# Kernel tuning notes

Hardware: AMD Instinct MI355X
Metric: run time of the kernel (lower is better)

The kernel has to match this reference:

```python
import jax, jax.numpy as jnp
import numpy as np

SAMPLE_RATE = 32000.0
NUM_APPLICATIONS = 3


def _eq_biquad(x, freq, gain, q, sr):
    """torchaudio.functional.equalizer_biquad: peaking EQ biquad + lfilter.
    x: [B, T] float; freq/gain/q: scalars.
    """
    w0 = 2.0 * jnp.pi * freq / sr
    A = jnp.exp(gain / 40.0 * jnp.log(10.0))  # 10 ** (gain / 40)
    alpha = jnp.sin(w0) / (2.0 * q)
    b0 = 1.0 + alpha * A
    b1 = -2.0 * jnp.cos(w0)
    b2 = 1.0 - alpha * A
    a0 = 1.0 + alpha / A
    a1 = -2.0 * jnp.cos(w0)
    a2 = 1.0 - alpha / A
    # normalize by a0 (as torchaudio biquad -> lfilter does)
    b0, b1, b2 = b0 / a0, b1 / a0, b2 / a0
    a1, a2 = a1 / a0, a2 / a0

    B = x.shape[0]
    z = jnp.zeros((B,), x.dtype)

    def step(carry, xn):
        x1, x2, y1, y2 = carry
        yn = b0 * xn + b1 * x1 + b2 * x2 - a1 * y1 - a2 * y2
        return (xn, x1, yn, y1), yn

    # scan over time axis; carry is per-batch state vectors
    _, y = jax.lax.scan(step, (z, z, z, z), x.T)  # y: [T, B]
    return y.T


def setup_inputs() -> dict:
    key = jax.random.key(0)
    k1, k2, k3, k4 = jax.random.split(key, 4)
    clip = jax.random.normal(k1, (128, 160000), dtype=jnp.float32)
    # draws within the module's f/g/q ranges
    freqs = jax.random.uniform(k2, (NUM_APPLICATIONS,), jnp.float32, 100.0, 6000.0)
    gains = jax.random.uniform(k3, (NUM_APPLICATIONS,), jnp.float32, -8.0, 8.0)
    qs = jax.random.uniform(k4, (NUM_APPLICATIONS,), jnp.float32, 1.0, 9.0)
    return {"clip": clip, "freqs": freqs, "gains": gains, "qs": qs}


def reference(clip, freqs, gains, qs):
    x = clip
    for i in range(NUM_APPLICATIONS):
        x = _eq_biquad(x, freqs[i], gains[i], qs[i], SAMPLE_RATE)
    return x
```

## Files before the change

### kernel.cpp

```cpp
#include <hip/hip_runtime.h>
#include <math.h>

#define SRATE 32000.f
#define NB 128
#define NT 160000
#define CL 50
#define CPB 128
#define NCROW 3200
#define NTILE 3200
#define TPR 25
#define SEG 50
#define LROW 52
#define RECROW (NCROW*8)

#ifndef M_PI
#define M_PI 3.14159265358979323846
#endif

__device__ __forceinline__ void coeffs_f32(
    const float* fr, const float* gn, const float* qs, float* c)
{
  #pragma unroll
  for (int f = 0; f < 3; ++f) {
    float w0 = 2.f * (float)M_PI * fr[f] / SRATE;
    float A  = expf(gn[f] * (2.302585093f / 40.f));
    float al = sinf(w0) / (2.f * qs[f]);
    float cw = cosf(w0);
    float a0 = 1.f + al / A;
    c[f*5+0] = (1.f + al*A) / a0;
    c[f*5+1] = -2.f * cw / a0;
    c[f*5+2] = (1.f - al*A) / a0;
    c[f*5+3] = -2.f * cw / a0;
    c[f*5+4] = (1.f - al/A) / a0;
  }
}


__global__ __launch_bounds__(128) void eq_a(
    const float* __restrict__ x, const float* __restrict__ fr,
    const float* __restrict__ gn, const float* __restrict__ qs,
    float* __restrict__ eoT)
{
  __shared__ float lds[CPB * LROW];
  const int tid = threadIdx.x;
  const int t = blockIdx.x;
  float c[15];
  coeffs_f32(fr, gn, qs, c);
  const float* xg = x + (size_t)t * (CPB * CL);
  #pragma unroll
  for (int it = 0; it < 25; ++it) {
    int f = it * 128 + tid;
    int seg = f / 25, off = f % 25;
    float2 v = *(const float2*)(xg + seg*CL + off*2);
    int pos = off + seg; pos -= (pos >= 25) ? 25 : 0; pos -= (pos >= 25) ? 25 : 0;
    pos = (off + seg) % 25;
    *(float2*)(&lds[seg*LROW + pos*2]) = v;
  }
  __syncthreads();
  const int gci = t * CPB + tid;
  const int ci  = gci % NCROW;
  float x1, x2;
  if (tid == 0) {
    if (ci == 0) { x1 = 0.f; x2 = 0.f; }
    else { x1 = xg[-1]; x2 = xg[-2]; }
  } else {
    const int ps = tid - 1;
    const int pp = (ps + 24) % 25;
    x1 = lds[ps*LROW + pp*2 + 1];
    x2 = lds[ps*LROW + pp*2 + 0];
  }
  float y1p=0,y1pp=0,y2p=0,y2pp=0,y3p=0,y3pp=0;
  int rr = tid % 25;
  #pragma unroll
  for (int jj = 0; jj < 25; ++jj) {
    float2 xv = *(const float2*)(&lds[tid*LROW + rr*2]);
    rr = (rr == 24) ? 0 : rr + 1;
    #pragma unroll
    for (int q = 0; q < 2; ++q) {
      const float xn = q ? xv.y : xv.x;
      float y1 = c[0]*xn + c[1]*x1  + c[2]*x2   - c[3]*y1p  - c[4]*y1pp;
      float y2 = c[5]*y1 + c[6]*y1p + c[7]*y1pp - c[8]*y2p  - c[9]*y2pp;
      float y3 = c[10]*y2 + c[11]*y2p + c[12]*y2pp - c[13]*y3p - c[14]*y3pp;
      x2=x1; x1=xn;
      y1pp=y1p; y1p=y1; y2pp=y2p; y2p=y2; y3pp=y3p; y3p=y3;
    }
  }
  const int row = gci / NCROW;
  const int plane = ci % SEG, slot = ci / SEG;
  float* ep = eoT + (size_t)row * RECROW + ((size_t)plane*64 + slot)*8;
  float4 r0; r0.x=y1p; r0.y=y1pp; r0.z=y2p; r0.w=y2pp;
  float4 r1; r1.x=y3p; r1.y=y3pp; r1.z=0.f; r1.w=0.f;
  *(float4*)ep = r0; *(float4*)(ep+4) = r1;
}

__global__ __launch_bounds__(64) void eq_b(
    const float* __restrict__ fr, const float* __restrict__ gn,
    const float* __restrict__ qs, const float* __restrict__ eoT,
    float* __restrict__ sgD)
{
  __shared__ double Mb[36], Rb[36], Tb[36];
  __shared__ float Hs[36], Gs[6*36];
  const int l = threadIdx.x, row = blockIdx.x;
  float c[15];
  coeffs_f32(fr, gn, qs, c);
  if (l < 6) {
    double s0=0,s1=0,s2=0,s3=0,s4=0,s5=0;
    if (l==0) s0=1; else if (l==1) s1=1; else if (l==2) s2=1;
    else if (l==3) s3=1; else if (l==4) s4=1; else s5=1;
    double y1 = -(double)c[3]*s0 - (double)c[4]*s1;
    double y2 = (double)c[5]*y1 + (double)c[6]*s0 + (double)c[7]*s1
              - (double)c[8]*s2 - (double)c[9]*s3;
    double y3 = (double)c[10]*y2 + (double)c[11]*s2 + (double)c[12]*s3
              - (double)c[13]*s4 - (double)c[14]*s5;
    Mb[0*6+l]=y1; Mb[1*6+l]=s0; Mb[2*6+l]=y2; Mb[3*6+l]=s2; Mb[4*6+l]=y3; Mb[5*6+l]=s4;
  }
  if (l < 36) Rb[l] = ((l % 7) == 0) ? 1.0 : 0.0;
  __syncthreads();
  const int i = l / 6, j = l % 6;
  int e = CL;
  while (e) {
    if (e & 1) {
      double acc = 0.0;
      if (l < 36) { for (int k = 0; k < 6; ++k) acc += Rb[i*6+k]*Mb[k*6+j]; Tb[l]=acc; }
      __syncthreads();
      if (l < 36) Rb[l] = Tb[l];
      __syncthreads();
    }
    e >>= 1;
    if (e) {
      double acc = 0.0;
      if (l < 36) { for (int k = 0; k < 6; ++k) acc += Mb[i*6+k]*Mb[k*6+j]; Tb[l]=acc; }
      __syncthreads();
      if (l < 36) Mb[l] = Tb[l];
      __syncthreads();
    }
  }
  if (l < 36) { Hs[l] = (float)Rb[l]; Mb[l] = Rb[l]; }
  __syncthreads();
  if (l < 36) Rb[l] = ((l % 7) == 0) ? 1.0 : 0.0;
  __syncthreads();
  e = SEG;
  while (e) {
    if (e & 1) {
      double acc = 0.0;
      if (l < 36) { for (int k = 0; k < 6; ++k) acc += Rb[i*6+k]*Mb[k*6+j]; Tb[l]=acc; }
      __syncthreads();
      if (l < 36) Rb[l] = Tb[l];
      __syncthreads();
    }
    e >>= 1;
    if (e) {
      double acc = 0.0;
      if (l < 36) { for (int k = 0; k < 6; ++k) acc += Mb[i*6+k]*Mb[k*6+j]; Tb[l]=acc; }
      __syncthreads();
      if (l < 36) Mb[l] = Tb[l];
      __syncthreads();
    }
  }
  if (l < 36) Gs[l] = (float)Rb[l];
  __syncthreads();
  for (int k = 1; k < 6; ++k) {
    double acc = 0.0;
    if (l < 36) { for (int m = 0; m < 6; ++m) acc += Rb[i*6+m]*Rb[m*6+j]; Tb[l]=acc; }
    __syncthreads();
    if (l < 36) Rb[l] = Tb[l];
    __syncthreads();
    if (l < 36) Gs[k*36+l] = (float)Rb[l];
    __syncthreads();
  }

  float H[36];
  #pragma unroll
  for (int q = 0; q < 36; ++q) H[q] = Hs[q];
  const float* rbase = eoT + (size_t)row * RECROW;
  float u[6] = {0,0,0,0,0,0};
  for (int jj = 0; jj < SEG; ++jj) {
    const float* ep = rbase + ((size_t)jj*64 + l)*8;
    float4 r0 = *(const float4*)ep, r1 = *(const float4*)(ep+4);
    float ev[6] = {r0.x,r0.y,r0.z,r0.w,r1.x,r1.y};
    float nu[6];
    #pragma unroll
    for (int q = 0; q < 6; ++q) {
      float a = ev[q];
      #pragma unroll
      for (int m = 0; m < 6; ++m) a += H[q*6+m]*u[m];
      nu[q] = a;
    }
    #pragma unroll
    for (int q = 0; q < 6; ++q) u[q] = nu[q];
  }
  float v6[6];
  #pragma unroll
  for (int q = 0; q < 6; ++q) v6[q] = u[q];
  #pragma unroll
  for (int k = 0; k < 6; ++k) {
    const float* G = Gs + k*36;
    float o[6];
    #pragma unroll
    for (int q = 0; q < 6; ++q) o[q] = __shfl_up(v6[q], 1u << k, 64);
    if (l >= (1 << k)) {
      float nv[6];
      #pragma unroll
      for (int q = 0; q < 6; ++q) {
        float a = v6[q];
        #pragma unroll
        for (int m = 0; m < 6; ++m) a += G[q*6+m]*o[m];
        nv[q] = a;
      }
      #pragma unroll
      for (int q = 0; q < 6; ++q) v6[q] = nv[q];
    }
  }
  float s[6];
  #pragma unroll
  for (int q = 0; q < 6; ++q) s[q] = __shfl_up(v6[q], 1, 64);
  if (l == 0) {
    #pragma unroll
    for (int q = 0; q < 6; ++q) s[q] = 0.f;
  }
  float* wbase = sgD + (size_t)row * RECROW;
  for (int jj = 0; jj < SEG; ++jj) {
    const float* ep = rbase + ((size_t)jj*64 + l)*8;
    float4 r0 = *(const float4*)ep, r1 = *(const float4*)(ep+4);
    float ev[6] = {r0.x,r0.y,r0.z,r0.w,r1.x,r1.y};
    float* wp = wbase + ((size_t)l*SEG + jj)*8;
    float4 w0; w0.x=s[0]; w0.y=s[1]; w0.z=s[2]; w0.w=s[3];
    float4 w1; w1.x=s[4]; w1.y=s[5]; w1.z=0.f; w1.w=0.f;
    *(float4*)wp = w0; *(float4*)(wp+4) = w1;
    float ns[6];
    #pragma unroll
    for (int q = 0; q < 6; ++q) {
      float a = ev[q];
      #pragma unroll
      for (int m = 0; m < 6; ++m) a += H[q*6+m]*s[m];
      ns[q] = a;
    }
    #pragma unroll
    for (int q = 0; q < 6; ++q) s[q] = ns[q];
  }
}

__global__ __launch_bounds__(128) void eq_c(
    const float* __restrict__ x, const float* __restrict__ fr,
    const float* __restrict__ gn, const float* __restrict__ qs,
    const float* __restrict__ sgD, float* __restrict__ y)
{
  __shared__ float lds[CPB * LROW];
  const int tid = threadIdx.x;
  const int t = blockIdx.x;
  float c[15];
  coeffs_f32(fr, gn, qs, c);
  const float* xg = x + (size_t)t * (CPB * CL);
  float* yg = y + (size_t)t * (CPB * CL);
  #pragma unroll
  for (int it = 0; it < 25; ++it) {
    int f = it * 128 + tid;
    int seg = f / 25, off = f % 25;
    float2 v = *(const float2*)(xg + seg*CL + off*2);
    int pos = (off + seg) % 25;
    *(float2*)(&lds[seg*LROW + pos*2]) = v;
  }
  __syncthreads();
  const int gci = t * CPB + tid;
  const int ci  = gci % NCROW;
  float x1, x2;
  if (tid == 0) {
    if (ci == 0) { x1 = 0.f; x2 = 0.f; }
    else { x1 = xg[-1]; x2 = xg[-2]; }
  } else {
    const int ps = tid - 1;
    const int pp = (ps + 24) % 25;
    x1 = lds[ps*LROW + pp*2 + 1];
    x2 = lds[ps*LROW + pp*2 + 0];
  }
  __syncthreads();
  const int row = gci / NCROW;
  const float* sp = sgD + (size_t)row * RECROW + (size_t)ci * 8;
  float4 s0 = *(const float4*)sp, s1 = *(const float4*)(sp+4);
  float y1p=s0.x, y1pp=s0.y, y2p=s0.z, y2pp=s0.w, y3p=s1.x, y3pp=s1.y;
  int rr = tid % 25;
  #pragma unroll
  for (int jj = 0; jj < 25; ++jj) {
    float2 xv = *(const float2*)(&lds[tid*LROW + rr*2]);
    float2 yv;
    #pragma unroll
    for (int q = 0; q < 2; ++q) {
      const float xn = q ? xv.y : xv.x;
      float y1 = c[0]*xn + c[1]*x1  + c[2]*x2   - c[3]*y1p  - c[4]*y1pp;
      float y2 = c[5]*y1 + c[6]*y1p + c[7]*y1pp - c[8]*y2p  - c[9]*y2pp;
      float y3 = c[10]*y2 + c[11]*y2p + c[12]*y2pp - c[13]*y3p - c[14]*y3pp;
      x2=x1; x1=xn;
      y1pp=y1p; y1p=y1; y2pp=y2p; y2p=y2; y3pp=y3p; y3p=y3;
      if (q) yv.y = y3; else yv.x = y3;
    }
    *(float2*)(&lds[tid*LROW + rr*2]) = yv;
    rr = (rr == 24) ? 0 : rr + 1;
  }
  __syncthreads();
  #pragma unroll
  for (int it = 0; it < 25; ++it) {
    int f = it * 128 + tid;
    int seg = f / 25, off = f % 25;
    int pos = (off + seg) % 25;
    float2 v = *(const float2*)(&lds[seg*LROW + pos*2]);
    *(float2*)(yg + seg*CL + off*2) = v;
  }
}

extern "C" void kernel_launch(void* const* d_in, const int* in_sizes, int n_in,
                              void* d_out, int out_size, void* d_ws, size_t ws_size,
                              hipStream_t stream) {
  const float* clip = (const float*)d_in[0];
  const float* fr   = (const float*)d_in[1];
  const float* gn   = (const float*)d_in[2];
  const float* qs   = (const float*)d_in[3];
  float* out = (float*)d_out;
  float* eoT = (float*)d_ws;
  float* sgD = eoT + (size_t)NB * RECROW;

  eq_a<<<NTILE, 128, 0, stream>>>(clip, fr, gn, qs, eoT);
  eq_b<<<NB, 64, 0, stream>>>(fr, gn, qs, eoT, sgD);
  eq_c<<<NTILE, 128, 0, stream>>>(clip, fr, gn, qs, sgD, out);
}
```

Measured before the change: 90.61 us.

## Persistent grid with double-buffered async global-to-LDS staging in scan kernels

Converts the two per-chunk IIR kernels into persistent kernels over a fixed grid that loop over tiles. Each next tile is prefetched into a second LDS buffer with direct global-to-LDS loads while the current tile is filtered. The swizzled padded LDS layout is replaced by a plain contiguous layout, and neighbour history is obtained with a wavefront shuffle instead of LDS reads. This aims to hide global load latency and cut staging instruction overhead, at the cost of possible LDS bank conflicts and reliance on correct async-load synchronization.

```diff
diff --git a/kernel.cpp b/kernel.cpp
--- a/kernel.cpp
+++ b/kernel.cpp
@@ -10,7 +10,8 @@
 #define NTILE 3200
 #define TPR 25
 #define SEG 50
-#define LROW 52
+#define TILEF 6400
+#define GRID 768
 #define RECROW (NCROW*8)
 
 #ifndef M_PI
@@ -35,62 +36,74 @@
   }
 }
 
+__device__ __forceinline__ void stage_half(
+    const float* __restrict__ src0, float* dst0, int lane)
+{
+  const float* src = src0 + lane * 4;
+  #pragma unroll
+  for (int cc = 0; cc < 12; ++cc) {
+    __builtin_amdgcn_global_load_lds(
+        (const __attribute__((address_space(1))) void*)(src + cc*256),
+        (__attribute__((address_space(3))) void*)(dst0 + cc*256), 16, 0, 0);
+  }
+  if (lane < 32) {
+    __builtin_amdgcn_global_load_lds(
+        (const __attribute__((address_space(1))) void*)(src + 12*256),
+        (__attribute__((address_space(3))) void*)(dst0 + 12*256), 16, 0, 0);
+  }
+}
 
 __global__ __launch_bounds__(128) void eq_a(
     const float* __restrict__ x, const float* __restrict__ fr,
     const float* __restrict__ gn, const float* __restrict__ qs,
     float* __restrict__ eoT)
 {
-  __shared__ float lds[CPB * LROW];
-  const int tid = threadIdx.x;
-  const int t = blockIdx.x;
+  __shared__ float lds[2][TILEF];
+  const int tid = threadIdx.x, lane = tid & 63, wave = tid >> 6;
   float c[15];
   coeffs_f32(fr, gn, qs, c);
-  const float* xg = x + (size_t)t * (CPB * CL);
-  #pragma unroll
-  for (int it = 0; it < 25; ++it) {
-    int f = it * 128 + tid;
-    int seg = f / 25, off = f % 25;
-    float2 v = *(const float2*)(xg + seg*CL + off*2);
-    int pos = off + seg; pos -= (pos >= 25) ? 25 : 0; pos -= (pos >= 25) ? 25 : 0;
-    pos = (off + seg) % 25;
-    *(float2*)(&lds[seg*LROW + pos*2]) = v;
-  }
-  __syncthreads();
-  const int gci = t * CPB + tid;
-  const int ci  = gci % NCROW;
-  float x1, x2;
-  if (tid == 0) {
-    if (ci == 0) { x1 = 0.f; x2 = 0.f; }
-    else { x1 = xg[-1]; x2 = xg[-2]; }
-  } else {
-    const int ps = tid - 1;
-    const int pp = (ps + 24) % 25;
-    x1 = lds[ps*LROW + pp*2 + 1];
-    x2 = lds[ps*LROW + pp*2 + 0];
-  }
-  float y1p=0,y1pp=0,y2p=0,y2pp=0,y3p=0,y3pp=0;
-  int rr = tid % 25;
-  #pragma unroll
-  for (int jj = 0; jj < 25; ++jj) {
-    float2 xv = *(const float2*)(&lds[tid*LROW + rr*2]);
-    rr = (rr == 24) ? 0 : rr + 1;
-    #pragma unroll
-    for (int q = 0; q < 2; ++q) {
-      const float xn = q ? xv.y : xv.x;
-      float y1 = c[0]*xn + c[1]*x1  + c[2]*x2   - c[3]*y1p  - c[4]*y1pp;
-      float y2 = c[5]*y1 + c[6]*y1p + c[7]*y1pp - c[8]*y2p  - c[9]*y2pp;
-      float y3 = c[10]*y2 + c[11]*y2p + c[12]*y2pp - c[13]*y3p - c[14]*y3pp;
-      x2=x1; x1=xn;
-      y1pp=y1p; y1p=y1; y2pp=y2p; y2p=y2; y3pp=y3p; y3p=y3;
-    }
-  }
-  const int row = gci / NCROW;
-  const int plane = ci % SEG, slot = ci / SEG;
-  float* ep = eoT + (size_t)row * RECROW + ((size_t)plane*64 + slot)*8;
-  float4 r0; r0.x=y1p; r0.y=y1pp; r0.z=y2p; r0.w=y2pp;
-  float4 r1; r1.x=y3p; r1.y=y3pp; r1.z=0.f; r1.w=0.f;
-  *(float4*)ep = r0; *(float4*)(ep+4) = r1;
+  const int b = blockIdx.x;
+  stage_half(x + (size_t)b*TILEF + wave*3200, &lds[0][wave*3200], lane);
+  __syncthreads();
+  int cur = 0;
+  for (int t = b; t < NTILE; t += GRID) {
+    const int tn = t + GRID;
+    if (tn < NTILE)
+      stage_half(x + (size_t)tn*TILEF + wave*3200, &lds[cur^1][wave*3200], lane);
+    const int gch = t*CPB + tid;
+    const int ci  = (t % TPR)*CPB + tid;
+    float bx1 = 0.f, bx2 = 0.f;
+    if (lane == 0 && ci != 0) {
+      const float* p = x + (size_t)gch * CL;
+      bx1 = p[-1]; bx2 = p[-2];
+    }
+    const float* myrow = &lds[cur][tid*CL];
+    float a48 = myrow[48], a49 = myrow[49];
+    float x1 = __shfl_up(a49, 1, 64), x2 = __shfl_up(a48, 1, 64);
+    if (lane == 0) { x1 = bx1; x2 = bx2; }
+    float y1p=0,y1pp=0,y2p=0,y2pp=0,y3p=0,y3pp=0;
+    #pragma unroll
+    for (int j = 0; j < 25; ++j) {
+      float2 xv = *(const float2*)(myrow + 2*j);
+      #pragma unroll
+      for (int q = 0; q < 2; ++q) {
+        const float xn = q ? xv.y : xv.x;
+        float y1 = c[0]*xn + c[1]*x1  + c[2]*x2   - c[3]*y1p  - c[4]*y1pp;
+        float y2 = c[5]*y1 + c[6]*y1p + c[7]*y1pp - c[8]*y2p  - c[9]*y2pp;
+        float y3 = c[10]*y2 + c[11]*y2p + c[12]*y2pp - c[13]*y3p - c[14]*y3pp;
+        x2=x1; x1=xn;
+        y1pp=y1p; y1p=y1; y2pp=y2p; y2p=y2; y3pp=y3p; y3p=y3;
+      }
+    }
+    const int row = t / TPR;
+    const int plane = ci % SEG, slot = ci / SEG;
+    float* ep = eoT + (size_t)row * RECROW + ((size_t)(plane*64 + slot))*8;
+    float4 r0; r0.x=y1p; r0.y=y1pp; r0.z=y2p; r0.w=y2pp;
+    float4 r1; r1.x=y3p; r1.y=y3pp; r1.z=0.f; r1.w=0.f;
+    *(float4*)ep = r0; *(float4*)(ep+4) = r1;
+    __syncthreads();
+    cur ^= 1;
+  }
 }
 
 __global__ __launch_bounds__(64) void eq_b(
@@ -245,65 +258,59 @@
     const float* __restrict__ gn, const float* __restrict__ qs,
     const float* __restrict__ sgD, float* __restrict__ y)
 {
-  __shared__ float lds[CPB * LROW];
-  const int tid = threadIdx.x;
-  const int t = blockIdx.x;
+  __shared__ float lds[2][TILEF];
+  const int tid = threadIdx.x, lane = tid & 63, wave = tid >> 6;
   float c[15];
   coeffs_f32(fr, gn, qs, c);
-  const float* xg = x + (size_t)t * (CPB * CL);
-  float* yg = y + (size_t)t * (CPB * CL);
-  #pragma unroll
-  for (int it = 0; it < 25; ++it) {
-    int f = it * 128 + tid;
-    int seg = f / 25, off = f % 25;
-    float2 v = *(const float2*)(xg + seg*CL + off*2);
-    int pos = (off + seg) % 25;
-    *(float2*)(&lds[seg*LROW + pos*2]) = v;
-  }
-  __syncthreads();
-  const int gci = t * CPB + tid;
-  const int ci  = gci % NCROW;
-  float x1, x2;
-  if (tid == 0) {
-    if (ci == 0) { x1 = 0.f; x2 = 0.f; }
-    else { x1 = xg[-1]; x2 = xg[-2]; }
-  } else {
-    const int ps = tid - 1;
-    const int pp = (ps + 24) % 25;
-    x1 = lds[ps*LROW + pp*2 + 1];
-    x2 = lds[ps*LROW + pp*2 + 0];
-  }
-  __syncthreads();
-  const int row = gci / NCROW;
-  const float* sp = sgD + (size_t)row * RECROW + (size_t)ci * 8;
-  float4 s0 = *(const float4*)sp, s1 = *(const float4*)(sp+4);
-  float y1p=s0.x, y1pp=s0.y, y2p=s0.z, y2pp=s0.w, y3p=s1.x, y3pp=s1.y;
-  int rr = tid % 25;
-  #pragma unroll
-  for (int jj = 0; jj < 25; ++jj) {
-    float2 xv = *(const float2*)(&lds[tid*LROW + rr*2]);
-    float2 yv;
-    #pragma unroll
-    for (int q = 0; q < 2; ++q) {
-      const float xn = q ? xv.y : xv.x;
-      float y1 = c[0]*xn + c[1]*x1  + c[2]*x2   - c[3]*y1p  - c[4]*y1pp;
-      float y2 = c[5]*y1 + c[6]*y1p + c[7]*y1pp - c[8]*y2p  - c[9]*y2pp;
-      float y3 = c[10]*y2 + c[11]*y2p + c[12]*y2pp - c[13]*y3p - c[14]*y3pp;
-      x2=x1; x1=xn;
-      y1pp=y1p; y1p=y1; y2pp=y2p; y2p=y2; y3pp=y3p; y3p=y3;
-      if (q) yv.y = y3; else yv.x = y3;
-    }
-    *(float2*)(&lds[tid*LROW + rr*2]) = yv;
-    rr = (rr == 24) ? 0 : rr + 1;
-  }
-  __syncthreads();
-  #pragma unroll
-  for (int it = 0; it < 25; ++it) {
-    int f = it * 128 + tid;
-    int seg = f / 25, off = f % 25;
-    int pos = (off + seg) % 25;
-    float2 v = *(const float2*)(&lds[seg*LROW + pos*2]);
-    *(float2*)(yg + seg*CL + off*2) = v;
+  const int b = blockIdx.x;
+  stage_half(x + (size_t)b*TILEF + wave*3200, &lds[0][wave*3200], lane);
+  __syncthreads();
+  int cur = 0;
+  for (int t = b; t < NTILE; t += GRID) {
+    const int tn = t + GRID;
+    if (tn < NTILE)
+      stage_half(x + (size_t)tn*TILEF + wave*3200, &lds[cur^1][wave*3200], lane);
+    const int gch = t*CPB + tid;
+    const int ci  = (t % TPR)*CPB + tid;
+    const int row = t / TPR;
+    float bx1 = 0.f, bx2 = 0.f;
+    if (lane == 0 && ci != 0) {
+      const float* p = x + (size_t)gch * CL;
+      bx1 = p[-1]; bx2 = p[-2];
+    }
+    const float* sp = sgD + (size_t)row * RECROW + (size_t)ci * 8;
+    float4 s0 = *(const float4*)sp, s1 = *(const float4*)(sp+4);
+    float* myrow = &lds[cur][tid*CL];
+    float a48 = myrow[48], a49 = myrow[49];
+    float x1 = __shfl_up(a49, 1, 64), x2 = __shfl_up(a48, 1, 64);
+    if (lane == 0) { x1 = bx1; x2 = bx2; }
+    float y1p=s0.x, y1pp=s0.y, y2p=s0.z, y2pp=s0.w, y3p=s1.x, y3pp=s1.y;
+    #pragma unroll
+    for (int j = 0; j < 25; ++j) {
+      float2 xv = *(const float2*)(myrow + 2*j);
+      float2 yv;
+      #pragma unroll
+      for (int q = 0; q < 2; ++q) {
+        const float xn = q ? xv.y : xv.x;
+        float y1 = c[0]*xn + c[1]*x1  + c[2]*x2   - c[3]*y1p  - c[4]*y1pp;
+        float y2 = c[5]*y1 + c[6]*y1p + c[7]*y1pp - c[8]*y2p  - c[9]*y2pp;
+        float y3 = c[10]*y2 + c[11]*y2p + c[12]*y2pp - c[13]*y3p - c[14]*y3pp;
+        x2=x1; x1=xn;
+        y1pp=y1p; y1p=y1; y2pp=y2p; y2p=y2; y3pp=y3p; y3p=y3;
+        if (q) yv.y = y3; else yv.x = y3;
+      }
+      *(float2*)(myrow + 2*j) = yv;
+    }
+    __syncthreads();
+    float* yg = y + (size_t)t * TILEF;
+    #pragma unroll
+    for (int it = 0; it < 25; ++it) {
+      int f = it * 128 + tid;
+      float2 v = *(const float2*)(&lds[cur][2*f]);
+      *(float2*)(yg + 2*f) = v;
+    }
+    __syncthreads();
+    cur ^= 1;
   }
 }
 
@@ -318,7 +325,7 @@
   float* eoT = (float*)d_ws;
   float* sgD = eoT + (size_t)NB * RECROW;
 
-  eq_a<<<NTILE, 128, 0, stream>>>(clip, fr, gn, qs, eoT);
+  eq_a<<<GRID, 128, 0, stream>>>(clip, fr, gn, qs, eoT);
   eq_b<<<NB, 64, 0, stream>>>(fr, gn, qs, eoT, sgD);
-  eq_c<<<NTILE, 128, 0, stream>>>(clip, fr, gn, qs, sgD, out);
-}
+  eq_c<<<GRID, 128, 0, stream>>>(clip, fr, gn, qs, sgD, out);
+}
```

New measurement: 76.55 us. 1.18x faster.
